# Kernel optimization log

Hardware: AMD Instinct MI355X
Metric: run time of the kernel (lower is better)

## Reference

```python
import jax, jax.numpy as jnp
import numpy as np

N = 16384
F_IN = 64
F_OUT = 64


def setup_inputs() -> dict:
    key = jax.random.key(0)
    k1, k2, k3 = jax.random.split(key, 3)
    x = jax.random.normal(k1, (N, F_IN), dtype=jnp.float32)
    # dense binary adjacency (what dense_to_sparse consumes)
    adj = jax.random.randint(k2, (N, N), 0, 2).astype(jnp.float32)
    W = jax.random.normal(k3, (F_IN, F_OUT), dtype=jnp.float32) * (1.0 / np.sqrt(F_IN))
    b = jnp.zeros((F_OUT,), dtype=jnp.float32)
    return {"x": x, "adj": adj, "W": W, "b": b}


def reference(x, adj, W, b):
    # GCNConv with edge_weight from dense_to_sparse(adj), add_self_loops=True,
    # symmetric normalization: out = D^{-1/2} A_hat^T D^{-1/2} (x W) + b,
    # where A_hat = adj + I and D is the column-degree of A_hat.
    # Dropout is identity in eval mode (training=False). Activation = relu.
    deg = adj.sum(axis=0) + 1.0                      # [N] col sums incl. self-loop
    dinv = jnp.where(deg > 0, jax.lax.rsqrt(deg), 0.0)
    xw = x @ W                                       # [N, F_OUT]
    z = dinv[:, None] * xw                           # scale by source deg^-1/2
    # A_hat^T @ z = adj^T @ z + z (self-loop term), avoids materializing A + I
    out = dinv[:, None] * (adj.T @ z + z) + b
    return jax.nn.relu(out)
```

## Files before the change

### kernel.cpp

```cpp
#include <hip/hip_runtime.h>
#include <cstdint>
#include <cstddef>

#define GN 16384
#define GF 64
#define NW (GN / 32)

typedef __bf16 bf16x8 __attribute__((ext_vector_type(8)));
typedef float f32x4 __attribute__((ext_vector_type(4)));
typedef unsigned int u32x4 __attribute__((ext_vector_type(4)));

__device__ __forceinline__ bf16x8 decode8(unsigned int b) {
  unsigned int t = (b & 0xffu) * 0x8001u;
  u32x4 r;
  r[0] = (t & 0x00010001u) * 0x3F80u;
  r[1] = ((t >> 2) & 0x00010001u) * 0x3F80u;
  r[2] = ((t >> 4) & 0x00010001u) * 0x3F80u;
  r[3] = ((t >> 6) & 0x00010001u) * 0x3F80u;
  return __builtin_bit_cast(bf16x8, r);
}

__device__ __forceinline__ unsigned short f2bf(float v) {
  unsigned int u = __builtin_bit_cast(unsigned int, v);
  u += 0x7fffu + ((u >> 16) & 1u);
  return (unsigned short)(u >> 16);
}

__device__ __forceinline__ float bf2f(unsigned short s) {
  return __builtin_bit_cast(float, (unsigned int)s << 16);
}

__global__ __launch_bounds__(256) void k_pack(const float* __restrict__ adj,
                                              float* __restrict__ deg,
                                              unsigned int* __restrict__ packed) {
  const int cb = blockIdx.x >> 5;
  const int jb = blockIdx.x & 31;
  const int col0 = cb * 1024 + threadIdx.x * 4;
  const int j0 = jb * 512;
  int cnt0 = 0, cnt1 = 0, cnt2 = 0, cnt3 = 0;

  u32x4 vv0[4], vv1[4], vv2[4], vv3[4];

#pragma unroll
  for (int seg = 0; seg < 4; ++seg) {
#pragma unroll
    for (int q = 0; q < 4; ++q) {
      unsigned int w0 = 0, w1 = 0, w2 = 0, w3 = 0;
      const float* base = adj + (size_t)(j0 + seg * 128 + q * 32) * GN + col0;
#pragma unroll 8
      for (int b = 0; b < 32; ++b) {
        f32x4 a = *(const f32x4*)(base + (size_t)b * GN);
        unsigned int m = 1u << b;
        if (a.x != 0.f) w0 |= m;
        if (a.y != 0.f) w1 |= m;
        if (a.z != 0.f) w2 |= m;
        if (a.w != 0.f) w3 |= m;
      }
      vv0[seg][q] = w0; vv1[seg][q] = w1; vv2[seg][q] = w2; vv3[seg][q] = w3;
      cnt0 += __popc(w0); cnt1 += __popc(w1); cnt2 += __popc(w2); cnt3 += __popc(w3);
    }
  }
#pragma unroll
  for (int seg = 0; seg < 4; ++seg) {
    unsigned int* q0 = packed + ((size_t)(jb * 4 + seg) * GN + col0) * 4;
    *(u32x4*)(q0 + 0)  = vv0[seg];
    *(u32x4*)(q0 + 4)  = vv1[seg];
    *(u32x4*)(q0 + 8)  = vv2[seg];
    *(u32x4*)(q0 + 12) = vv3[seg];
  }

  atomicAdd(&deg[col0 + 0], (float)cnt0);
  atomicAdd(&deg[col0 + 1], (float)cnt1);
  atomicAdd(&deg[col0 + 2], (float)cnt2);
  atomicAdd(&deg[col0 + 3], (float)cnt3);
}

__global__ __launch_bounds__(256) void k_z(const float* __restrict__ x,
                                           const float* __restrict__ W,
                                           const float* __restrict__ deg,
                                           float* __restrict__ dinv,
                                           unsigned short* __restrict__ z_rm,
                                           unsigned short* __restrict__ z2) {
  __shared__ float Wl[64][64];
  __shared__ float xl[64][64];
  const int tid = threadIdx.x;
  const int f = tid & 63;
  const int w = tid >> 6;
  const int rowB = blockIdx.x * 64;

  for (int idx = tid; idx < 4096; idx += 256) {
    Wl[idx >> 6][idx & 63] = W[idx];
    xl[idx >> 6][idx & 63] = x[(size_t)rowB * 64 + idx];
  }
  __syncthreads();

  float acc[16];
#pragma unroll
  for (int r = 0; r < 16; ++r) acc[r] = 0.f;
  for (int k = 0; k < 64; ++k) {
    float wk = Wl[k][f];
#pragma unroll
    for (int r = 0; r < 16; ++r) acc[r] = fmaf(xl[w * 16 + r][k], wk, acc[r]);
  }

  const int row0 = rowB + w * 16;
  if (f < 16) {
    int row = row0 + f;
    dinv[row] = 1.0f / sqrtf(deg[row] + 1.0f);
  }

  unsigned short zs[16];
#pragma unroll
  for (int r = 0; r < 16; ++r) {
    int row = row0 + r;
    float di = 1.0f / sqrtf(deg[row] + 1.0f);
    unsigned short zb = f2bf(di * acc[r]);
    zs[r] = zb;
    z_rm[(size_t)row * GF + f] = zb;
  }
  unsigned int p[8];
#pragma unroll
  for (int i = 0; i < 8; ++i)
    p[i] = (unsigned int)zs[2 * i] | ((unsigned int)zs[2 * i + 1] << 16);
  char* dst = (char*)z2 + (size_t)((rowB >> 5) + (w >> 1)) * 4096 +
              (f >> 4) * 1024 + ((2 * (w & 1)) * 16 + (f & 15)) * 16;
  u32x4 lo = {p[0], p[1], p[2], p[3]};
  u32x4 hi = {p[4], p[5], p[6], p[7]};
  *(u32x4*)dst = lo;
  *(u32x4*)(dst + 256) = hi;
}

__global__ __launch_bounds__(512) void k_spmm(const unsigned int* __restrict__ packed,
                                              const unsigned short* __restrict__ z2,
                                              const unsigned short* __restrict__ z_rm,
                                              const float* __restrict__ dinv,
                                              const float* __restrict__ bias,
                                              float* __restrict__ out) {
  __shared__ float red[4][64][64];
  const int i0 = blockIdx.x * 64;
  const int tid = threadIdx.x;
  const int wid = tid >> 6, lane = tid & 63;
  const int lrow = lane & 15, kb = lane >> 4;
  const int sh = kb * 8;

  f32x4 acc[4][4];
#pragma unroll
  for (int m = 0; m < 4; ++m)
#pragma unroll
    for (int n = 0; n < 4; ++n) acc[m][n] = (f32x4){0.f, 0.f, 0.f, 0.f};

  const size_t qstep = (size_t)GN * 4;
  const unsigned int* pr0 = packed + (size_t)(wid * 16) * qstep / 4 * 4 +
                            (size_t)(i0 + 0 * 16 + lrow) * 4;
  const unsigned int* pr1 = packed + (size_t)(wid * 16) * qstep / 4 * 4 +
                            (size_t)(i0 + 1 * 16 + lrow) * 4;
  const unsigned int* pr2 = packed + (size_t)(wid * 16) * qstep / 4 * 4 +
                            (size_t)(i0 + 2 * 16 + lrow) * 4;
  const unsigned int* pr3 = packed + (size_t)(wid * 16) * qstep / 4 * 4 +
                            (size_t)(i0 + 3 * 16 + lrow) * 4;
  const char* zbase = (const char*)z2 + (size_t)(wid * 64) * 4096 + lane * 16;

  bf16x8 cur0 = *(const bf16x8*)(zbase + 0 * 1024);
  bf16x8 cur1 = *(const bf16x8*)(zbase + 1 * 1024);
  bf16x8 cur2 = *(const bf16x8*)(zbase + 2 * 1024);
  bf16x8 cur3 = *(const bf16x8*)(zbase + 3 * 1024);
  u32x4 bits0 = *(const u32x4*)pr0;
  u32x4 bits1 = *(const u32x4*)pr1;
  u32x4 bits2 = *(const u32x4*)pr2;
  u32x4 bits3 = *(const u32x4*)pr3;

  for (int it = 0; it < 16; ++it) {
    u32x4 nb0 = *(const u32x4*)(pr0 + qstep);
    u32x4 nb1 = *(const u32x4*)(pr1 + qstep);
    u32x4 nb2 = *(const u32x4*)(pr2 + qstep);
    u32x4 nb3 = *(const u32x4*)(pr3 + qstep);
#pragma unroll
    for (int s = 0; s < 4; ++s) {
      const char* zn = zbase + (s + 1) * 4096;
      bf16x8 n0 = *(const bf16x8*)(zn + 0 * 1024);
      bf16x8 n1 = *(const bf16x8*)(zn + 1 * 1024);
      bf16x8 n2 = *(const bf16x8*)(zn + 2 * 1024);
      bf16x8 n3 = *(const bf16x8*)(zn + 3 * 1024);

      __builtin_amdgcn_s_setprio(1);
      bf16x8 a0 = decode8(bits0[s] >> sh);
      acc[0][0] = __builtin_amdgcn_mfma_f32_16x16x32_bf16(a0, cur0, acc[0][0], 0, 0, 0);
      acc[0][1] = __builtin_amdgcn_mfma_f32_16x16x32_bf16(a0, cur1, acc[0][1], 0, 0, 0);
      acc[0][2] = __builtin_amdgcn_mfma_f32_16x16x32_bf16(a0, cur2, acc[0][2], 0, 0, 0);
      acc[0][3] = __builtin_amdgcn_mfma_f32_16x16x32_bf16(a0, cur3, acc[0][3], 0, 0, 0);
      bf16x8 a1 = decode8(bits1[s] >> sh);
      acc[1][0] = __builtin_amdgcn_mfma_f32_16x16x32_bf16(a1, cur0, acc[1][0], 0, 0, 0);
      acc[1][1] = __builtin_amdgcn_mfma_f32_16x16x32_bf16(a1, cur1, acc[1][1], 0, 0, 0);
      acc[1][2] = __builtin_amdgcn_mfma_f32_16x16x32_bf16(a1, cur2, acc[1][2], 0, 0, 0);
      acc[1][3] = __builtin_amdgcn_mfma_f32_16x16x32_bf16(a1, cur3, acc[1][3], 0, 0, 0);
      bf16x8 a2 = decode8(bits2[s] >> sh);
      acc[2][0] = __builtin_amdgcn_mfma_f32_16x16x32_bf16(a2, cur0, acc[2][0], 0, 0, 0);
      acc[2][1] = __builtin_amdgcn_mfma_f32_16x16x32_bf16(a2, cur1, acc[2][1], 0, 0, 0);
      acc[2][2] = __builtin_amdgcn_mfma_f32_16x16x32_bf16(a2, cur2, acc[2][2], 0, 0, 0);
      acc[2][3] = __builtin_amdgcn_mfma_f32_16x16x32_bf16(a2, cur3, acc[2][3], 0, 0, 0);
      bf16x8 a3 = decode8(bits3[s] >> sh);
      acc[3][0] = __builtin_amdgcn_mfma_f32_16x16x32_bf16(a3, cur0, acc[3][0], 0, 0, 0);
      acc[3][1] = __builtin_amdgcn_mfma_f32_16x16x32_bf16(a3, cur1, acc[3][1], 0, 0, 0);
      acc[3][2] = __builtin_amdgcn_mfma_f32_16x16x32_bf16(a3, cur2, acc[3][2], 0, 0, 0);
      acc[3][3] = __builtin_amdgcn_mfma_f32_16x16x32_bf16(a3, cur3, acc[3][3], 0, 0, 0);
      __builtin_amdgcn_s_setprio(0);

      cur0 = n0; cur1 = n1; cur2 = n2; cur3 = n3;
    }
    bits0 = nb0; bits1 = nb1; bits2 = nb2; bits3 = nb3;
    pr0 += qstep; pr1 += qstep; pr2 += qstep; pr3 += qstep;
    zbase += 16384;
  }

  if (wid < 4) {
#pragma unroll
    for (int m = 0; m < 4; ++m)
#pragma unroll
      for (int n = 0; n < 4; ++n)
#pragma unroll
        for (int r = 0; r < 4; ++r)
          red[wid][m * 16 + kb * 4 + r][n * 16 + lrow] = acc[m][n][r];
  }
  __syncthreads();
  if (wid >= 4) {
#pragma unroll
    for (int m = 0; m < 4; ++m)
#pragma unroll
      for (int n = 0; n < 4; ++n)
#pragma unroll
        for (int r = 0; r < 4; ++r)
          red[wid - 4][m * 16 + kb * 4 + r][n * 16 + lrow] += acc[m][n][r];
  }
  __syncthreads();

  const int c = tid & 63;
  const int rg = tid >> 6;
  const float bc = bias[c];
#pragma unroll
  for (int rr = 0; rr < 8; ++rr) {
    int r = rg * 8 + rr;
    int i = i0 + r;
    float s = red[0][r][c] + red[1][r][c] + red[2][r][c] + red[3][r][c];
    float o = dinv[i] * (s + bf2f(z_rm[(size_t)i * GF + c])) + bc;
    out[(size_t)i * GF + c] = fmaxf(o, 0.f);
  }
}

extern "C" void kernel_launch(void* const* d_in, const int* in_sizes, int n_in,
                              void* d_out, int out_size, void* d_ws, size_t ws_size,
                              hipStream_t stream) {
  const float* x = (const float*)d_in[0];
  const float* adj = (const float*)d_in[1];
  const float* W = (const float*)d_in[2];
  const float* bias = (const float*)d_in[3];
  float* out = (float*)d_out;

  char* ws = (char*)d_ws;
  float* deg = (float*)ws;
  float* dinv = (float*)(ws + 65536);
  unsigned short* z_rm = (unsigned short*)(ws + 131072);
  unsigned short* z2 = (unsigned short*)(ws + 131072 + 2097152);
  unsigned int* packed = (unsigned int*)(ws + 131072 + 4194304);
  if (ws_size < 38928384u) return;

  hipMemsetAsync(deg, 0, GN * sizeof(float), stream);
  k_pack<<<dim3(512), dim3(256), 0, stream>>>(adj, deg, packed);
  k_z<<<dim3(GN / 64), dim3(256), 0, stream>>>(x, W, deg, dinv, z_rm, z2);
  k_spmm<<<dim3(GN / 64), dim3(512), 0, stream>>>(packed, z2, z_rm, dinv, bias, out);
}
```

Baseline: 237.5 us.

## Restructure adjacency packing tiles and replace degree atomics with per-block byte counts

```diff
diff --git a/kernel.cpp b/kernel.cpp
--- a/kernel.cpp
+++ b/kernel.cpp
@@ -31,58 +31,78 @@
 }
 
 __global__ __launch_bounds__(256) void k_pack(const float* __restrict__ adj,
-                                              float* __restrict__ deg,
+                                              unsigned char* __restrict__ cnt8,
                                               unsigned int* __restrict__ packed) {
-  const int cb = blockIdx.x >> 5;
-  const int jb = blockIdx.x & 31;
-  const int col0 = cb * 1024 + threadIdx.x * 4;
-  const int j0 = jb * 512;
-  int cnt0 = 0, cnt1 = 0, cnt2 = 0, cnt3 = 0;
-
-  u32x4 vv0[4], vv1[4], vv2[4], vv3[4];
-
-#pragma unroll
-  for (int seg = 0; seg < 4; ++seg) {
-#pragma unroll
-    for (int q = 0; q < 4; ++q) {
-      unsigned int w0 = 0, w1 = 0, w2 = 0, w3 = 0;
-      const float* base = adj + (size_t)(j0 + seg * 128 + q * 32) * GN + col0;
-#pragma unroll 8
-      for (int b = 0; b < 32; ++b) {
-        f32x4 a = *(const f32x4*)(base + (size_t)b * GN);
-        unsigned int m = 1u << b;
-        if (a.x != 0.f) w0 |= m;
-        if (a.y != 0.f) w1 |= m;
-        if (a.z != 0.f) w2 |= m;
-        if (a.w != 0.f) w3 |= m;
+  const int cb = blockIdx.x >> 7;
+  const int jb = blockIdx.x & 127;
+  const int col0 = cb * 4096 + (int)threadIdx.x * 4;
+  const int j0 = jb * 128;
+
+  u32x4 wq[4][4];
+#pragma unroll
+  for (int cc = 0; cc < 4; ++cc)
+#pragma unroll
+    for (int j = 0; j < 4; ++j) wq[cc][j] = (u32x4){0u, 0u, 0u, 0u};
+
+#pragma unroll
+  for (int q = 0; q < 4; ++q) {
+    unsigned int w[4][4];
+#pragma unroll
+    for (int cc = 0; cc < 4; ++cc)
+#pragma unroll
+      for (int j = 0; j < 4; ++j) w[cc][j] = 0u;
+#pragma unroll 4
+    for (int b = 0; b < 32; ++b) {
+      const float* rowp = adj + (size_t)(j0 + q * 32 + b) * GN + col0;
+      const unsigned int m = 1u << b;
+#pragma unroll
+      for (int cc = 0; cc < 4; ++cc) {
+        f32x4 a = *(const f32x4*)(rowp + cc * 1024);
+        if (a.x != 0.f) w[cc][0] |= m;
+        if (a.y != 0.f) w[cc][1] |= m;
+        if (a.z != 0.f) w[cc][2] |= m;
+        if (a.w != 0.f) w[cc][3] |= m;
       }
-      vv0[seg][q] = w0; vv1[seg][q] = w1; vv2[seg][q] = w2; vv3[seg][q] = w3;
-      cnt0 += __popc(w0); cnt1 += __popc(w1); cnt2 += __popc(w2); cnt3 += __popc(w3);
     }
-  }
-#pragma unroll
-  for (int seg = 0; seg < 4; ++seg) {
-    unsigned int* q0 = packed + ((size_t)(jb * 4 + seg) * GN + col0) * 4;
-    *(u32x4*)(q0 + 0)  = vv0[seg];
-    *(u32x4*)(q0 + 4)  = vv1[seg];
-    *(u32x4*)(q0 + 8)  = vv2[seg];
-    *(u32x4*)(q0 + 12) = vv3[seg];
-  }
-
-  atomicAdd(&deg[col0 + 0], (float)cnt0);
-  atomicAdd(&deg[col0 + 1], (float)cnt1);
-  atomicAdd(&deg[col0 + 2], (float)cnt2);
-  atomicAdd(&deg[col0 + 3], (float)cnt3);
+#pragma unroll
+    for (int cc = 0; cc < 4; ++cc)
+#pragma unroll
+      for (int j = 0; j < 4; ++j) wq[cc][j][q] = w[cc][j];
+  }
+
+#pragma unroll
+  for (int cc = 0; cc < 4; ++cc) {
+    unsigned int* q0 = packed + ((size_t)jb * GN + col0 + cc * 1024) * 4;
+    *(u32x4*)(q0 + 0)  = wq[cc][0];
+    *(u32x4*)(q0 + 4)  = wq[cc][1];
+    *(u32x4*)(q0 + 8)  = wq[cc][2];
+    *(u32x4*)(q0 + 12) = wq[cc][3];
+  }
+
+#pragma unroll
+  for (int cc = 0; cc < 4; ++cc) {
+    unsigned int c0 = __popc(wq[cc][0][0]) + __popc(wq[cc][0][1]) +
+                      __popc(wq[cc][0][2]) + __popc(wq[cc][0][3]);
+    unsigned int c1 = __popc(wq[cc][1][0]) + __popc(wq[cc][1][1]) +
+                      __popc(wq[cc][1][2]) + __popc(wq[cc][1][3]);
+    unsigned int c2 = __popc(wq[cc][2][0]) + __popc(wq[cc][2][1]) +
+                      __popc(wq[cc][2][2]) + __popc(wq[cc][2][3]);
+    unsigned int c3 = __popc(wq[cc][3][0]) + __popc(wq[cc][3][1]) +
+                      __popc(wq[cc][3][2]) + __popc(wq[cc][3][3]);
+    *(unsigned int*)(cnt8 + (size_t)jb * GN + col0 + cc * 1024) =
+        c0 | (c1 << 8) | (c2 << 16) | (c3 << 24);
+  }
 }
 
 __global__ __launch_bounds__(256) void k_z(const float* __restrict__ x,
                                            const float* __restrict__ W,
-                                           const float* __restrict__ deg,
+                                           const unsigned char* __restrict__ cnt8,
                                            float* __restrict__ dinv,
                                            unsigned short* __restrict__ z_rm,
                                            unsigned short* __restrict__ z2) {
   __shared__ float Wl[64][64];
   __shared__ float xl[64][64];
+  __shared__ float degl[64];
   const int tid = threadIdx.x;
   const int f = tid & 63;
   const int w = tid >> 6;
@@ -92,6 +112,12 @@
     Wl[idx >> 6][idx & 63] = W[idx];
     xl[idx >> 6][idx & 63] = x[(size_t)rowB * 64 + idx];
   }
+  if (tid < 64) {
+    int s = 1;
+    for (int jbb = 0; jbb < 128; ++jbb)
+      s += (int)cnt8[(size_t)jbb * GN + rowB + tid];
+    degl[tid] = (float)s;
+  }
   __syncthreads();
 
   float acc[16];
@@ -106,17 +132,16 @@
   const int row0 = rowB + w * 16;
   if (f < 16) {
     int row = row0 + f;
-    dinv[row] = 1.0f / sqrtf(deg[row] + 1.0f);
+    dinv[row] = 1.0f / sqrtf(degl[w * 16 + f]);
   }
 
   unsigned short zs[16];
 #pragma unroll
   for (int r = 0; r < 16; ++r) {
-    int row = row0 + r;
-    float di = 1.0f / sqrtf(deg[row] + 1.0f);
+    float di = 1.0f / sqrtf(degl[w * 16 + r]);
     unsigned short zb = f2bf(di * acc[r]);
     zs[r] = zb;
-    z_rm[(size_t)row * GF + f] = zb;
+    z_rm[(size_t)(row0 + r) * GF + f] = zb;
   }
   unsigned int p[8];
 #pragma unroll
@@ -256,15 +281,14 @@
   float* out = (float*)d_out;
 
   char* ws = (char*)d_ws;
-  float* deg = (float*)ws;
-  float* dinv = (float*)(ws + 65536);
-  unsigned short* z_rm = (unsigned short*)(ws + 131072);
-  unsigned short* z2 = (unsigned short*)(ws + 131072 + 2097152);
-  unsigned int* packed = (unsigned int*)(ws + 131072 + 4194304);
-  if (ws_size < 38928384u) return;
-
-  hipMemsetAsync(deg, 0, GN * sizeof(float), stream);
-  k_pack<<<dim3(512), dim3(256), 0, stream>>>(adj, deg, packed);
-  k_z<<<dim3(GN / 64), dim3(256), 0, stream>>>(x, W, deg, dinv, z_rm, z2);
+  unsigned char* cnt8 = (unsigned char*)ws;
+  float* dinv = (float*)(ws + 2097152);
+  unsigned short* z_rm = (unsigned short*)(ws + 2097152 + 65536);
+  unsigned short* z2 = (unsigned short*)(ws + 4194304 + 65536);
+  unsigned int* packed = (unsigned int*)(ws + 6291456 + 65536);
+  if (ws_size < 40435712u) return;
+
+  k_pack<<<dim3(512), dim3(256), 0, stream>>>(adj, cnt8, packed);
+  k_z<<<dim3(GN / 64), dim3(256), 0, stream>>>(x, W, cnt8, dinv, z_rm, z2);
   k_spmm<<<dim3(GN / 64), dim3(512), 0, stream>>>(packed, z2, z_rm, dinv, bias, out);
 }
```

Measured after the change: 239.9 us. About the same (+1.0%).
